# Kernel tuning notes

Measured on AMD Instinct MI355X. Metric: run time of the kernel, lower is better.

The kernel has to match this reference:

```python
import jax, jax.numpy as jnp
import numpy as np

N, D_IN, D_OUT, H, E = 8192, 1024, 1024, 1024, 8
EPS = 0.2
S_FACTOR = 5.0


def setup_inputs() -> dict:
    key = jax.random.key(0)
    k0, k1, k2, k3 = jax.random.split(key, 4)
    x = jax.random.normal(k0, (N, D_IN), jnp.float32)
    # selector Linear(nIn, E); weights scaled by sFactor as in SMoE.__init__
    Wsel = jax.random.normal(k1, (D_IN, E), jnp.float32) * (S_FACTOR / np.sqrt(D_IN))
    bsel = jnp.zeros((E,), jnp.float32)
    # stacked 2-layer MLP experts: Linear(D_IN,H) -> ReLU -> Linear(H,D_OUT)
    W1 = jax.random.normal(k2, (E, D_IN, H), jnp.float32) / np.sqrt(D_IN)
    b1 = jnp.zeros((E, H), jnp.float32)
    W2 = jax.random.normal(k3, (E, H, D_OUT), jnp.float32) / np.sqrt(H)
    b2 = jnp.zeros((E, D_OUT), jnp.float32)
    return {"x": x, "Wsel": Wsel, "bsel": bsel, "W1": W1, "b1": b1, "W2": W2, "b2": b2}


def _sparse_weights(weightMat):
    # sort experts per token, descending (torch.sort(..., 1, descending=True))
    order = jnp.argsort(-weightMat, axis=1)                # [N,E]
    topW = jnp.take_along_axis(weightMat, order, axis=1)
    cumW = jnp.cumsum(topW, axis=1)
    capped = jnp.minimum(cumW, 1.0 - EPS)
    sw_sorted = jax.nn.relu(capped - cumW + topW)          # sparse weights, sorted order
    # softCost (side-effect metric in the original; not returned by SMoE.forward)
    shifted = jnp.pad(sw_sorted[:, 1:], ((0, 0), (0, 1)))
    _soft_cost = jnp.sum(jnp.where(shifted > 0, 1.0, sw_sorted), axis=1)
    # faithful to torch.gather(sparse_weight, 1, index) in the source
    sw = jnp.take_along_axis(sw_sorted, order, axis=1)     # [N,E]
    return sw


def reference(x, Wsel, bsel, W1, b1, W2, b2):
    weightMat = jax.nn.softmax(x @ Wsel + bsel, axis=1)    # [N,E] selector
    sw = _sparse_weights(weightMat)                        # [N,E] sparse combine weights
    # dense (vectorized) expert dispatch: tokens with sw==0 contribute 0,
    # numerically identical to the gather/scatter_add loop in sparse_MoE
    h = jax.nn.relu(jnp.einsum('nd,edh->enh', x, W1) + b1[:, None, :])   # [E,N,H]
    y = jnp.einsum('enh,eho->eno', h, W2) + b2[:, None, :]               # [E,N,O]
    out = jnp.einsum('ne,eno->no', sw, y)                                # [N,O]
    return out
```

## Files before the change

### kernel.cpp

```cpp
#include <hip/hip_runtime.h>
#include <hip/hip_bf16.h>
#include <stdint.h>

#define N_TOK 8192
#define DIN   1024
#define DOUT  1024
#define HID   1024
#define NE    8
#define CAP   0.8f

typedef __attribute__((ext_vector_type(8))) short short8;
typedef __attribute__((ext_vector_type(4))) float floatx4;

__device__ __forceinline__ void async_load16(const void* g, void* l) {
  __builtin_amdgcn_global_load_lds(
      (const __attribute__((address_space(1))) void*)g,
      (__attribute__((address_space(3))) void*)l,
      16, 0, 0);
}

__device__ __forceinline__ unsigned short bf16_bits(float f) {
  return __builtin_bit_cast(unsigned short, __float2bfloat16(f));
}

__global__ __launch_bounds__(256) void selector_kernel(
    const float* __restrict__ x, const float* __restrict__ Wsel,
    const float* __restrict__ bsel,
    __hip_bfloat16* __restrict__ x_bf, float* __restrict__ sw,
    float4* __restrict__ out4)
{
  {
    const int base = blockIdx.x * 4096 + threadIdx.x;
    const float4 z4 = {0.f, 0.f, 0.f, 0.f};
#pragma unroll
    for (int r = 0; r < 16; r++) out4[base + r * 256] = z4;
  }

  const int lane = threadIdx.x & 63;
  const int wave = threadIdx.x >> 6;
  const int tok0 = blockIdx.x * 16 + wave * 4;
  const float* xr = x + (size_t)tok0 * DIN;
  const float4* W4 = (const float4*)Wsel;

  float acc[4][8];
#pragma unroll
  for (int m = 0; m < 4; m++)
#pragma unroll
    for (int e = 0; e < 8; e++) acc[m][e] = 0.f;

#pragma unroll
  for (int i = 0; i < 16; i++) {
    const int d = lane + i * 64;
    const float4 wlo = W4[d * 2];
    const float4 whi = W4[d * 2 + 1];
#pragma unroll
    for (int m = 0; m < 4; m++) {
      const float xv = xr[m * DIN + d];
      acc[m][0] += xv * wlo.x; acc[m][1] += xv * wlo.y;
      acc[m][2] += xv * wlo.z; acc[m][3] += xv * wlo.w;
      acc[m][4] += xv * whi.x; acc[m][5] += xv * whi.y;
      acc[m][6] += xv * whi.z; acc[m][7] += xv * whi.w;
    }
  }
#pragma unroll
  for (int off = 32; off >= 1; off >>= 1)
#pragma unroll
    for (int m = 0; m < 4; m++)
#pragma unroll
      for (int e = 0; e < 8; e++) acc[m][e] += __shfl_xor(acc[m][e], off);

  if (lane < 4) {
    const int n = tok0 + lane;
    float w[8];
    float mx = -1e30f;
#pragma unroll
    for (int e = 0; e < 8; e++) { w[e] = acc[lane][e] + bsel[e]; mx = fmaxf(mx, w[e]); }
    float s = 0.f;
#pragma unroll
    for (int e = 0; e < 8; e++) { w[e] = expf(w[e] - mx); s += w[e]; }
    const float inv = 1.f / s;
#pragma unroll
    for (int e = 0; e < 8; e++) w[e] *= inv;

    float wsrt[8]; int ord[8];
    for (int k = 0; k < 8; k++) {
      const float v = w[k];
      int j = k;
      while (j > 0 && wsrt[j - 1] < v) { wsrt[j] = wsrt[j - 1]; ord[j] = ord[j - 1]; j--; }
      wsrt[j] = v; ord[j] = k;
    }
    float cum = 0.f, sws[8];
    for (int k = 0; k < 8; k++) {
      cum += wsrt[k];
      const float capped = fminf(cum, CAP);
      sws[k] = fmaxf(capped - cum + wsrt[k], 0.f);
    }
    for (int j = 0; j < 8; j++) sw[(size_t)n * 8 + j] = sws[ord[j]];
  }

  const float4* xr4 = (const float4*)xr;
  ushort4* xb4 = (ushort4*)(x_bf + (size_t)tok0 * DIN);
#pragma unroll
  for (int m = 0; m < 4; m++)
#pragma unroll
    for (int i = 0; i < 4; i++) {
      const int d4 = lane + i * 64;
      const float4 xv = xr4[m * 256 + d4];
      ushort4 p;
      p.x = bf16_bits(xv.x);
      p.y = bf16_bits(xv.y);
      p.z = bf16_bits(xv.z);
      p.w = bf16_bits(xv.w);
      xb4[m * 256 + d4] = p;
    }
}

__global__ __launch_bounds__(1024) void compact_convert_kernel(
    const float* __restrict__ sw, int* __restrict__ idx, int* __restrict__ cnt,
    const float* __restrict__ W1, const float* __restrict__ W2,
    __hip_bfloat16* __restrict__ W1t, __hip_bfloat16* __restrict__ W2t)
{
  const int z = blockIdx.z;
  const int t = threadIdx.x;

  if (z == 16) {
    const int bid = blockIdx.x + 16 * blockIdx.y;
    if (bid >= 8) return;
    const int e = bid;
    const int lane = t & 63;
    const int wv = t >> 6;
    __shared__ int wave_base[16];
    __shared__ int chunk_total;
    int base = 0;
#pragma unroll
    for (int c = 0; c < 8; c++) {
      const int tok = c * 1024 + t;
      const bool act = sw[(size_t)tok * 8 + e] > 0.f;
      const unsigned long long m = __ballot(act);
      const int before = __popcll(m & ((1ull << lane) - 1ull));
      if (lane == 0) wave_base[wv] = __popcll(m);
      __syncthreads();
      if (t == 0) {
        int s = 0;
        for (int w = 0; w < 16; w++) { const int v = wave_base[w]; wave_base[w] = s; s += v; }
        chunk_total = s;
      }
      __syncthreads();
      if (act) idx[e * N_TOK + base + wave_base[wv] + before] = tok;
      base += chunk_total;
      __syncthreads();
    }
    if (t == 0) cnt[e] = base;
    return;
  }

  __shared__ unsigned short tile[64][65];
  const float* src = (z & 8) ? W2 : W1;
  __hip_bfloat16* dst = (z & 8) ? W2t : W1t;
  const int e = z & 7;
  src += (size_t)e * 1024 * 1024;
  unsigned short* dstu = (unsigned short*)dst + (size_t)e * 1024 * 1024;
  const int R = blockIdx.y * 64, C = blockIdx.x * 64;

  {
    const int row = t >> 4;
    const int col4 = t & 15;
    const float4 v = *(const float4*)(src + (size_t)(R + row) * 1024 + C + col4 * 4);
    tile[row][col4 * 4 + 0] = bf16_bits(v.x);
    tile[row][col4 * 4 + 1] = bf16_bits(v.y);
    tile[row][col4 * 4 + 2] = bf16_bits(v.z);
    tile[row][col4 * 4 + 3] = bf16_bits(v.w);
  }
  __syncthreads();
  {
    const int d = t >> 4;
    const int j = t & 15;
    ushort4 o;
    o.x = tile[j * 4 + 0][d];
    o.y = tile[j * 4 + 1][d];
    o.z = tile[j * 4 + 2][d];
    o.w = tile[j * 4 + 3][d];
    *(ushort4*)(dstu + (size_t)(C + d) * 1024 + R + j * 4) = o;
  }
}

#define BUFO (128 * 32)

template <int MODE>
__global__ __launch_bounds__(256, 2) void moe_gemm(
    const __hip_bfloat16* __restrict__ x_bf,
    __hip_bfloat16* __restrict__ hpool,
    const __hip_bfloat16* __restrict__ Wt,
    const float* __restrict__ biasAll,
    const float* __restrict__ sw,
    const int* __restrict__ idx, const int* __restrict__ cnt,
    float* __restrict__ out)
{
  const int e = blockIdx.z;
  const int count = cnt[e];
  const int m0 = blockIdx.y * 128;
  if (m0 >= count) return;
  const int n0 = blockIdx.x * 128;

  __shared__ __align__(16) __hip_bfloat16 sA[2 * BUFO];
  __shared__ __align__(16) __hip_bfloat16 sB[2 * BUFO];
  const int t = threadIdx.x;
  const int lane = t & 63;
  const int wave = t >> 6;
  const int wm = (wave & 1) * 64;
  const int wn = (wave >> 1) * 64;
  const int* idx_e = idx + e * N_TOK;
  const float* bias = biasAll + e * 1024;

  floatx4 acc[4][4];
#pragma unroll
  for (int i = 0; i < 4; i++)
#pragma unroll
    for (int j = 0; j < 4; j++) acc[i][j] = (floatx4){0.f, 0.f, 0.f, 0.f};

  const int sr = t >> 2;
  const int sc = (t & 3) * 8;
  const __hip_bfloat16* Ag0;
  const __hip_bfloat16* Ag1;
  if (MODE == 0) {
    const int t0 = idx_e[min(m0 + sr, count - 1)];
    const int t1 = idx_e[min(m0 + sr + 64, count - 1)];
    Ag0 = x_bf + (size_t)t0 * 1024 + sc;
    Ag1 = x_bf + (size_t)t1 * 1024 + sc;
  } else {
    const __hip_bfloat16* hp = hpool + (size_t)e * N_TOK * 1024;
    Ag0 = hp + (size_t)(m0 + sr) * 1024 + sc;
    Ag1 = hp + (size_t)(m0 + sr + 64) * 1024 + sc;
  }
  const __hip_bfloat16* Bg = Wt + (size_t)e * 1024 * 1024 + (size_t)(n0 + sr) * 1024 + sc;
  __hip_bfloat16* lA = &sA[sr * 32 + sc];
  __hip_bfloat16* lB = &sB[sr * 32 + sc];

  const int rf = lane & 15;
  const int k8 = (lane >> 4) * 8;
  const int roA = (wm + rf) * 32 + k8;
  const int roB = (wn + rf) * 32 + k8;

  async_load16(Ag0, lA);
  async_load16(Ag1, lA + 64 * 32);
  async_load16(Bg, lB);
  async_load16(Bg + (size_t)64 * 1024, lB + 64 * 32);
  __syncthreads();

#define STEP(KT, RB, WB)                                                        \
  {                                                                             \
    const int knext = ((KT) + 1) * 32;                                          \
    if (knext < 1024) {                                                         \
      async_load16(Ag0 + knext, lA + (WB) * BUFO);                              \
      async_load16(Ag1 + knext, lA + (WB) * BUFO + 64 * 32);                    \
      async_load16(Bg + knext, lB + (WB) * BUFO);                               \
      async_load16(Bg + (size_t)64 * 1024 + knext, lB + (WB) * BUFO + 64 * 32); \
    }                                                                           \
    const __hip_bfloat16* pA = &sA[(RB) * BUFO + roA];                          \
    const __hip_bfloat16* pB = &sB[(RB) * BUFO + roB];                          \
    short8 aF[4], bF[4];                                                        \
    _Pragma("unroll")                                                           \
    for (int i = 0; i < 4; i++) aF[i] = *(const short8*)(pA + i * 16 * 32);     \
    _Pragma("unroll")                                                           \
    for (int j = 0; j < 4; j++) bF[j] = *(const short8*)(pB + j * 16 * 32);     \
    _Pragma("unroll")                                                           \
    for (int i = 0; i < 4; i++)                                                 \
      _Pragma("unroll")                                                         \
      for (int j = 0; j < 4; j++)                                               \
        acc[i][j] = __builtin_amdgcn_mfma_f32_16x16x32_bf16(aF[i], bF[j],       \
                                                            acc[i][j], 0, 0, 0);\
    __syncthreads();                                                            \
  }

  for (int kt = 0; kt < 32; kt += 2) {
    STEP(kt, 0, 1);
    STEP(kt + 1, 1, 0);
  }
#undef STEP

  const int quad = lane >> 4;
  const int cn = lane & 15;
#pragma unroll
  for (int i = 0; i < 4; i++) {
#pragma unroll
    for (int r = 0; r < 4; r++) {
      const int gm = m0 + wm + i * 16 + quad * 4 + r;
      if (gm >= count) continue;
      int tok = 0; float swv = 0.f;
      if (MODE == 1) {
        tok = idx_e[gm];
        swv = sw[tok * 8 + e];
      }
#pragma unroll
      for (int j = 0; j < 4; j++) {
        const int gn = n0 + wn + j * 16 + cn;
        const float v = acc[i][j][r] + bias[gn];
        if (MODE == 0) {
          hpool[((size_t)e * N_TOK + gm) * 1024 + gn] = __float2bfloat16(fmaxf(v, 0.f));
        } else {
          unsafeAtomicAdd(&out[(size_t)tok * 1024 + gn], swv * v);
        }
      }
    }
  }
}

extern "C" void kernel_launch(void* const* d_in, const int* in_sizes, int n_in,
                              void* d_out, int out_size, void* d_ws, size_t ws_size,
                              hipStream_t stream) {
  const float* x    = (const float*)d_in[0];
  const float* Wsel = (const float*)d_in[1];
  const float* bsel = (const float*)d_in[2];
  const float* W1   = (const float*)d_in[3];
  const float* b1   = (const float*)d_in[4];
  const float* W2   = (const float*)d_in[5];
  const float* b2   = (const float*)d_in[6];
  float* out = (float*)d_out;

  char* ws = (char*)d_ws;
  __hip_bfloat16* x_bf = (__hip_bfloat16*)ws; ws += (size_t)N_TOK * DIN * 2;
  __hip_bfloat16* W1t  = (__hip_bfloat16*)ws; ws += (size_t)NE * DIN * HID * 2;
  __hip_bfloat16* W2t  = (__hip_bfloat16*)ws; ws += (size_t)NE * HID * DOUT * 2;
  float* sw            = (float*)ws;          ws += (size_t)N_TOK * NE * 4;
  int* idx             = (int*)ws;            ws += (size_t)NE * N_TOK * 4;
  int* cnt             = (int*)ws;            ws += 256;
  __hip_bfloat16* hpool = (__hip_bfloat16*)ws;

  selector_kernel<<<N_TOK / 16, 256, 0, stream>>>(x, Wsel, bsel, x_bf, sw,
                                                  (float4*)out);
  compact_convert_kernel<<<dim3(16, 16, 17), 1024, 0, stream>>>(
      sw, idx, cnt, W1, W2, W1t, W2t);

  moe_gemm<0><<<dim3(HID / 128, N_TOK / 128, NE), 256, 0, stream>>>(
      x_bf, hpool, W1t, b1, sw, idx, cnt, out);
  moe_gemm<1><<<dim3(DOUT / 128, N_TOK / 128, NE), 256, 0, stream>>>(
      x_bf, hpool, W2t, b2, sw, idx, cnt, out);
}
```

Baseline: 296.0 us.

## Triple-buffer LDS tiles with two-stage prefetch and vmcnt-based waits

Grows the shared-memory A/B tile buffers from two stages to three, so global-to-LDS loads run two K-steps ahead of the MFMA compute. The full __syncthreads is replaced by an explicit s_waitcnt vmcnt plus a bare s_barrier, so loads for the next stage can stay in flight across iterations. MFMA sections are bracketed with s_setprio to favour the math wave. The aim is to hide global load latency and barrier stalls, at the cost of more LDS per block. There is a risk that LDS data written by other threads is read before a barrier confirms it has landed.

```diff
diff --git a/kernel.cpp b/kernel.cpp
--- a/kernel.cpp
+++ b/kernel.cpp
@@ -202,8 +202,8 @@
   if (m0 >= count) return;
   const int n0 = blockIdx.x * 128;
 
-  __shared__ __align__(16) __hip_bfloat16 sA[2 * BUFO];
-  __shared__ __align__(16) __hip_bfloat16 sB[2 * BUFO];
+  __shared__ __align__(16) __hip_bfloat16 sA[3 * BUFO];
+  __shared__ __align__(16) __hip_bfloat16 sB[3 * BUFO];
   const int t = threadIdx.x;
   const int lane = t & 63;
   const int wave = t >> 6;
@@ -241,21 +241,19 @@
   const int roA = (wm + rf) * 32 + k8;
   const int roB = (wn + rf) * 32 + k8;
 
-  async_load16(Ag0, lA);
-  async_load16(Ag1, lA + 64 * 32);
-  async_load16(Bg, lB);
-  async_load16(Bg + (size_t)64 * 1024, lB + 64 * 32);
-  __syncthreads();
-
-#define STEP(KT, RB, WB)                                                        \
+#define STAGE(KT, WB)                                                           \
   {                                                                             \
-    const int knext = ((KT) + 1) * 32;                                          \
-    if (knext < 1024) {                                                         \
-      async_load16(Ag0 + knext, lA + (WB) * BUFO);                              \
-      async_load16(Ag1 + knext, lA + (WB) * BUFO + 64 * 32);                    \
-      async_load16(Bg + knext, lB + (WB) * BUFO);                               \
-      async_load16(Bg + (size_t)64 * 1024 + knext, lB + (WB) * BUFO + 64 * 32); \
-    }                                                                           \
+    const int kof = (KT) * 32;                                                  \
+    async_load16(Ag0 + kof, lA + (WB) * BUFO);                                  \
+    async_load16(Ag1 + kof, lA + (WB) * BUFO + 64 * 32);                        \
+    async_load16(Bg + kof, lB + (WB) * BUFO);                                   \
+    async_load16(Bg + (size_t)64 * 1024 + kof, lB + (WB) * BUFO + 64 * 32);     \
+  }
+
+#define P2ITER(KT, RB, WB, WAIT, DOSTAGE)                                       \
+  {                                                                             \
+    if (DOSTAGE) STAGE((KT) + 2, WB);                                           \
+    asm volatile("s_waitcnt " WAIT ::: "memory");                               \
     const __hip_bfloat16* pA = &sA[(RB) * BUFO + roA];                          \
     const __hip_bfloat16* pB = &sB[(RB) * BUFO + roB];                          \
     short8 aF[4], bF[4];                                                        \
@@ -263,20 +261,32 @@
     for (int i = 0; i < 4; i++) aF[i] = *(const short8*)(pA + i * 16 * 32);     \
     _Pragma("unroll")                                                           \
     for (int j = 0; j < 4; j++) bF[j] = *(const short8*)(pB + j * 16 * 32);     \
+    __builtin_amdgcn_s_setprio(1);                                              \
     _Pragma("unroll")                                                           \
     for (int i = 0; i < 4; i++)                                                 \
       _Pragma("unroll")                                                         \
       for (int j = 0; j < 4; j++)                                               \
         acc[i][j] = __builtin_amdgcn_mfma_f32_16x16x32_bf16(aF[i], bF[j],       \
                                                             acc[i][j], 0, 0, 0);\
-    __syncthreads();                                                            \
-  }
-
-  for (int kt = 0; kt < 32; kt += 2) {
-    STEP(kt, 0, 1);
-    STEP(kt + 1, 1, 0);
-  }
-#undef STEP
+    __builtin_amdgcn_s_setprio(0);                                              \
+    __builtin_amdgcn_s_barrier();                                               \
+  }
+
+  STAGE(0, 0);
+  STAGE(1, 1);
+  asm volatile("s_waitcnt vmcnt(4)" ::: "memory");
+  __builtin_amdgcn_s_barrier();
+
+#pragma unroll 1
+  for (int kt = 0; kt < 30; kt += 3) {
+    P2ITER(kt,     0, 2, "vmcnt(4)", true);
+    P2ITER(kt + 1, 1, 0, "vmcnt(4)", true);
+    P2ITER(kt + 2, 2, 1, "vmcnt(4)", true);
+  }
+  P2ITER(30, 0, 0, "vmcnt(0)", false);
+  P2ITER(31, 1, 0, "vmcnt(0)", false);
+#undef P2ITER
+#undef STAGE
 
   const int quad = lane >> 4;
   const int cn = lane & 15;
```

New measurement: 319.7 us. 8.0% more time.

## Use persistent grid-stride tile scheduler over active expert tiles in MoE GEMMs

Applied to the files above, without the earlier changes.

Replaces the dense 3D grid (8x64x8 blocks, most exiting early when beyond an expert's token count) with a 1D grid of 1024 blocks that loop over only the active tiles. The tiles come from a prefix sum of per-expert tile counts. The compaction block is also moved to z=0 so it gets scheduled first, ahead of the weight conversion blocks. This removes the launch and exit overhead of many empty blocks and balances work across CUs. The cost is a prefix sum computed per block and a loop that reuses shared memory across tiles.

```diff
diff --git a/kernel.cpp b/kernel.cpp
--- a/kernel.cpp
+++ b/kernel.cpp
@@ -123,7 +123,7 @@
   const int z = blockIdx.z;
   const int t = threadIdx.x;
 
-  if (z == 16) {
+  if (z == 0) {
     const int bid = blockIdx.x + 16 * blockIdx.y;
     if (bid >= 8) return;
     const int e = bid;
@@ -154,10 +154,11 @@
     return;
   }
 
+  const int zz = z - 1;
   __shared__ unsigned short tile[64][65];
-  const float* src = (z & 8) ? W2 : W1;
-  __hip_bfloat16* dst = (z & 8) ? W2t : W1t;
-  const int e = z & 7;
+  const float* src = (zz & 8) ? W2 : W1;
+  __hip_bfloat16* dst = (zz & 8) ? W2t : W1t;
+  const int e = zz & 7;
   src += (size_t)e * 1024 * 1024;
   unsigned short* dstu = (unsigned short*)dst + (size_t)e * 1024 * 1024;
   const int R = blockIdx.y * 64, C = blockIdx.x * 64;
@@ -196,109 +197,127 @@
     const int* __restrict__ idx, const int* __restrict__ cnt,
     float* __restrict__ out)
 {
-  const int e = blockIdx.z;
-  const int count = cnt[e];
-  const int m0 = blockIdx.y * 128;
-  if (m0 >= count) return;
-  const int n0 = blockIdx.x * 128;
-
   __shared__ __align__(16) __hip_bfloat16 sA[2 * BUFO];
   __shared__ __align__(16) __hip_bfloat16 sB[2 * BUFO];
+
+  int pref[NE + 1];
+  {
+    int tot = 0;
+#pragma unroll
+    for (int ee = 0; ee < NE; ee++) {
+      pref[ee] = tot;
+      tot += ((cnt[ee] + 127) >> 7) * 8;
+    }
+    pref[NE] = tot;
+  }
+  const int total = pref[NE];
+
   const int t = threadIdx.x;
   const int lane = t & 63;
   const int wave = t >> 6;
   const int wm = (wave & 1) * 64;
   const int wn = (wave >> 1) * 64;
-  const int* idx_e = idx + e * N_TOK;
-  const float* bias = biasAll + e * 1024;
-
-  floatx4 acc[4][4];
-#pragma unroll
-  for (int i = 0; i < 4; i++)
-#pragma unroll
-    for (int j = 0; j < 4; j++) acc[i][j] = (floatx4){0.f, 0.f, 0.f, 0.f};
-
   const int sr = t >> 2;
   const int sc = (t & 3) * 8;
-  const __hip_bfloat16* Ag0;
-  const __hip_bfloat16* Ag1;
-  if (MODE == 0) {
-    const int t0 = idx_e[min(m0 + sr, count - 1)];
-    const int t1 = idx_e[min(m0 + sr + 64, count - 1)];
-    Ag0 = x_bf + (size_t)t0 * 1024 + sc;
-    Ag1 = x_bf + (size_t)t1 * 1024 + sc;
-  } else {
-    const __hip_bfloat16* hp = hpool + (size_t)e * N_TOK * 1024;
-    Ag0 = hp + (size_t)(m0 + sr) * 1024 + sc;
-    Ag1 = hp + (size_t)(m0 + sr + 64) * 1024 + sc;
-  }
-  const __hip_bfloat16* Bg = Wt + (size_t)e * 1024 * 1024 + (size_t)(n0 + sr) * 1024 + sc;
-  __hip_bfloat16* lA = &sA[sr * 32 + sc];
-  __hip_bfloat16* lB = &sB[sr * 32 + sc];
-
   const int rf = lane & 15;
   const int k8 = (lane >> 4) * 8;
   const int roA = (wm + rf) * 32 + k8;
   const int roB = (wn + rf) * 32 + k8;
-
-  async_load16(Ag0, lA);
-  async_load16(Ag1, lA + 64 * 32);
-  async_load16(Bg, lB);
-  async_load16(Bg + (size_t)64 * 1024, lB + 64 * 32);
-  __syncthreads();
+  __hip_bfloat16* lA = &sA[sr * 32 + sc];
+  __hip_bfloat16* lB = &sB[sr * 32 + sc];
+
+  for (int w = blockIdx.x; w < total; w += gridDim.x) {
+    int e = 0;
+#pragma unroll
+    for (int ee = 1; ee < NE; ee++) if (w >= pref[ee]) e = ee;
+    const int local = w - pref[e];
+    const int m0 = (local >> 3) * 128;
+    const int n0 = (local & 7) * 128;
+    const int count = cnt[e];
+    const int* idx_e = idx + e * N_TOK;
+    const float* bias = biasAll + e * 1024;
+
+    floatx4 acc[4][4];
+#pragma unroll
+    for (int i = 0; i < 4; i++)
+#pragma unroll
+      for (int j = 0; j < 4; j++) acc[i][j] = (floatx4){0.f, 0.f, 0.f, 0.f};
+
+    const __hip_bfloat16* Ag0;
+    const __hip_bfloat16* Ag1;
+    if (MODE == 0) {
+      const int t0 = idx_e[min(m0 + sr, count - 1)];
+      const int t1 = idx_e[min(m0 + sr + 64, count - 1)];
+      Ag0 = x_bf + (size_t)t0 * 1024 + sc;
+      Ag1 = x_bf + (size_t)t1 * 1024 + sc;
+    } else {
+      const __hip_bfloat16* hp = hpool + (size_t)e * N_TOK * 1024;
+      Ag0 = hp + (size_t)(m0 + sr) * 1024 + sc;
+      Ag1 = hp + (size_t)(m0 + sr + 64) * 1024 + sc;
+    }
+    const __hip_bfloat16* Bg = Wt + (size_t)e * 1024 * 1024 +
+                               (size_t)(n0 + sr) * 1024 + sc;
+
+    async_load16(Ag0, lA);
+    async_load16(Ag1, lA + 64 * 32);
+    async_load16(Bg, lB);
+    async_load16(Bg + (size_t)64 * 1024, lB + 64 * 32);
+    __syncthreads();
 
 #define STEP(KT, RB, WB)                                                        \
-  {                                                                             \
-    const int knext = ((KT) + 1) * 32;                                          \
-    if (knext < 1024) {                                                         \
-      async_load16(Ag0 + knext, lA + (WB) * BUFO);                              \
-      async_load16(Ag1 + knext, lA + (WB) * BUFO + 64 * 32);                    \
-      async_load16(Bg + knext, lB + (WB) * BUFO);                               \
-      async_load16(Bg + (size_t)64 * 1024 + knext, lB + (WB) * BUFO + 64 * 32); \
-    }                                                                           \
-    const __hip_bfloat16* pA = &sA[(RB) * BUFO + roA];                          \
-    const __hip_bfloat16* pB = &sB[(RB) * BUFO + roB];                          \
-    short8 aF[4], bF[4];                                                        \
-    _Pragma("unroll")                                                           \
-    for (int i = 0; i < 4; i++) aF[i] = *(const short8*)(pA + i * 16 * 32);     \
-    _Pragma("unroll")                                                           \
-    for (int j = 0; j < 4; j++) bF[j] = *(const short8*)(pB + j * 16 * 32);     \
-    _Pragma("unroll")                                                           \
-    for (int i = 0; i < 4; i++)                                                 \
+    {                                                                           \
+      const int knext = ((KT) + 1) * 32;                                        \
+      if (knext < 1024) {                                                       \
+        async_load16(Ag0 + knext, lA + (WB) * BUFO);                            \
+        async_load16(Ag1 + knext, lA + (WB) * BUFO + 64 * 32);                  \
+        async_load16(Bg + knext, lB + (WB) * BUFO);                             \
+        async_load16(Bg + (size_t)64 * 1024 + knext, lB + (WB) * BUFO + 64*32); \
+      }                                                                         \
+      const __hip_bfloat16* pA = &sA[(RB) * BUFO + roA];                        \
+      const __hip_bfloat16* pB = &sB[(RB) * BUFO + roB];                        \
+      short8 aF[4], bF[4];                                                      \
       _Pragma("unroll")                                                         \
-      for (int j = 0; j < 4; j++)                                               \
-        acc[i][j] = __builtin_amdgcn_mfma_f32_16x16x32_bf16(aF[i], bF[j],       \
-                                                            acc[i][j], 0, 0, 0);\
-    __syncthreads();                                                            \
-  }
-
-  for (int kt = 0; kt < 32; kt += 2) {
-    STEP(kt, 0, 1);
-    STEP(kt + 1, 1, 0);
-  }
+      for (int i = 0; i < 4; i++) aF[i] = *(const short8*)(pA + i * 16 * 32);   \
+      _Pragma("unroll")                                                         \
+      for (int j = 0; j < 4; j++) bF[j] = *(const short8*)(pB + j * 16 * 32);   \
+      _Pragma("unroll")                                                         \
+      for (int i = 0; i < 4; i++)                                               \
+        _Pragma("unroll")                                                       \
+        for (int j = 0; j < 4; j++)                                             \
+          acc[i][j] = __builtin_amdgcn_mfma_f32_16x16x32_bf16(aF[i], bF[j],     \
+                                                              acc[i][j], 0,0,0);\
+      __syncthreads();                                                          \
+    }
+
+    for (int kt = 0; kt < 32; kt += 2) {
+      STEP(kt, 0, 1);
+      STEP(kt + 1, 1, 0);
+    }
 #undef STEP
 
-  const int quad = lane >> 4;
-  const int cn = lane & 15;
-#pragma unroll
-  for (int i = 0; i < 4; i++) {
-#pragma unroll
-    for (int r = 0; r < 4; r++) {
-      const int gm = m0 + wm + i * 16 + quad * 4 + r;
-      if (gm >= count) continue;
-      int tok = 0; float swv = 0.f;
-      if (MODE == 1) {
-        tok = idx_e[gm];
-        swv = sw[tok * 8 + e];
-      }
-#pragma unroll
-      for (int j = 0; j < 4; j++) {
-        const int gn = n0 + wn + j * 16 + cn;
-        const float v = acc[i][j][r] + bias[gn];
-        if (MODE == 0) {
-          hpool[((size_t)e * N_TOK + gm) * 1024 + gn] = __float2bfloat16(fmaxf(v, 0.f));
-        } else {
-          unsafeAtomicAdd(&out[(size_t)tok * 1024 + gn], swv * v);
+    const int quad = lane >> 4;
+    const int cn = lane & 15;
+#pragma unroll
+    for (int i = 0; i < 4; i++) {
+#pragma unroll
+      for (int r = 0; r < 4; r++) {
+        const int gm = m0 + wm + i * 16 + quad * 4 + r;
+        if (gm >= count) continue;
+        int tok = 0; float swv = 0.f;
+        if (MODE == 1) {
+          tok = idx_e[gm];
+          swv = sw[tok * 8 + e];
+        }
+#pragma unroll
+        for (int j = 0; j < 4; j++) {
+          const int gn = n0 + wn + j * 16 + cn;
+          const float v = acc[i][j][r] + bias[gn];
+          if (MODE == 0) {
+            hpool[((size_t)e * N_TOK + gm) * 1024 + gn] =
+                __float2bfloat16(fmaxf(v, 0.f));
+          } else {
+            unsafeAtomicAdd(&out[(size_t)tok * 1024 + gn], swv * v);
+          }
         }
       }
     }
@@ -331,8 +350,8 @@
   compact_convert_kernel<<<dim3(16, 16, 17), 1024, 0, stream>>>(
       sw, idx, cnt, W1, W2, W1t, W2t);
 
-  moe_gemm<0><<<dim3(HID / 128, N_TOK / 128, NE), 256, 0, stream>>>(
+  moe_gemm<0><<<1024, 256, 0, stream>>>(
       x_bf, hpool, W1t, b1, sw, idx, cnt, out);
-  moe_gemm<1><<<dim3(DOUT / 128, N_TOK / 128, NE), 256, 0, stream>>>(
+  moe_gemm<1><<<1024, 256, 0, stream>>>(
       x_bf, hpool, W2t, b2, sw, idx, cnt, out);
 }
```

Measured after the change: 300.8 us. About the same (+1.6%).
